# Performance work log

Measured on AMD Instinct MI355X. Metric: run time of the kernel, lower is better.

Reference implementation:

```python
import jax, jax.numpy as jnp
import numpy as np

ANISO = (0.096, 0.096, 0.096)
BIG = 1e10  # stands in for +inf feature distance
SMOOTH = 1e-05


def _minplus(f, axis, w):
    # exact 1D squared distance transform along `axis` via min-plus conv:
    # g[i] = min_j f[j] + (w*(i-j))^2 ; vectorized over all other dims.
    f = jnp.moveaxis(f, axis, -1)
    n = f.shape[-1]
    idx = jnp.arange(n, dtype=f.dtype)
    d2 = (w * (idx[:, None] - idx[None, :])) ** 2  # [j, i]
    g = jnp.min(f[..., :, None] + d2, axis=-2)
    return jnp.moveaxis(g, -1, axis)


def _edt_multilabel(labels, num_labels):
    # labels: [b, X, Y, Z] int, values in [1, num_labels]
    # Multi-label euclidean distance transform (edt.edt semantics on gt+1):
    # for each voxel, distance to nearest voxel carrying a DIFFERENT label,
    # scaled by ANISO. Computed as per-label squared EDT fields (separable
    # min-plus per axis, exact) combined by excluding the voxel's own label.
    fields = []
    for L in range(1, num_labels + 1):  # small fixed loop over classes
        f = jnp.where(labels == L, 0.0, BIG).astype(jnp.float32)
        for ax, w in zip((1, 2, 3), ANISO):
            f = _minplus(f, ax, w)
        fields.append(f)
    D = jnp.stack(fields, axis=0)  # [L, b, X, Y, Z] squared distances
    own = jnp.moveaxis(jax.nn.one_hot(labels - 1, num_labels, dtype=jnp.float32), -1, 0)
    d2 = jnp.min(jnp.where(own > 0, BIG, D), axis=0)  # nearest different label
    return jnp.sqrt(d2)


def setup_inputs() -> dict:
    key = jax.random.key(0)
    kx, ky = jax.random.split(key)
    x = jax.random.uniform(kx, (2, 3, 64, 64, 64), dtype=jnp.float32)  # softmax probs
    y = jax.random.randint(ky, (2, 1, 64, 64, 64), 0, 3)  # label map, classes 0..2
    return {"x": x, "y": y}


def reference(x, y):
    b, c = x.shape[:2]
    yi = y[:, 0]  # [b, X, Y, Z]
    # scatter_(1, gt, 1) -> one hot over channel dim
    y_onehot = jnp.moveaxis(jax.nn.one_hot(yi, c, dtype=x.dtype), -1, 1)  # [b,c,X,Y,Z]
    # dt = edt(gt + 1) + 1 ; all labels >=1 so every voxel is 'foreground'
    dt = (_edt_multilabel(yi + 1, c) + 1.0)[:, None]  # [b,1,X,Y,Z]
    fp = x * (1.0 - y_onehot) * dt
    fn = (1.0 - x) * y_onehot * dt
    # do_bg=False (non-batch-dice path): drop background channel
    fp = fp[:, 1:]
    fn = fn[:, 1:]
    return jnp.mean(fp) + jnp.mean(fn) + SMOOTH
```

## Files before the change

### kernel.cpp

```cpp
#include <hip/hip_runtime.h>
#include <math.h>

#define BIGV 10000000000.0f
#define WA   0.096f


__global__ __launch_bounds__(256) void pass_z_kernel(const int* __restrict__ lab,
                                                     float* __restrict__ D) {
    const int vol = blockIdx.y;
    const int b   = vol / 3;
    const int L   = vol % 3;
    const int ys  = blockIdx.x;
    const int lane = threadIdx.x & 63;
    const int wv   = threadIdx.x >> 6;

    __shared__ float s[64][64];

    const int* lp = lab + b * 262144 + ys * 64;
    for (int z = wv; z < 64; z += 4)
        s[z][lane] = (lp[z * 4096 + lane] == L) ? 0.0f : BIGV;
    __syncthreads();

    const int ibase = wv * 16;
    float m[16];
#pragma unroll
    for (int ii = 0; ii < 16; ++ii) m[ii] = __builtin_inff();

    for (int j = 0; j < 64; ++j) {
        const float v  = s[j][lane];
        const float fb = (float)(ibase - j);
#pragma unroll
        for (int ii = 0; ii < 16; ++ii) {
            const float t = WA * (fb + (float)ii);
            m[ii] = fminf(m[ii], __builtin_fmaf(t, t, v));
        }
    }

    float* Dp = D + vol * 262144 + ys * 64;
#pragma unroll
    for (int ii = 0; ii < 16; ++ii)
        Dp[(ibase + ii) * 4096 + lane] = m[ii];
}

__global__ __launch_bounds__(256) void pass_y_kernel(float* __restrict__ D) {
    const int vol = blockIdx.y;
    const int z   = blockIdx.x;
    const int lane = threadIdx.x & 63;
    const int wv   = threadIdx.x >> 6;

    __shared__ float s[64][64];
    float* Dp = D + (vol * 64 + z) * 4096;
    float* sf = &s[0][0];
    for (int t = threadIdx.x; t < 4096; t += 256) sf[t] = Dp[t];
    __syncthreads();

    const int ibase = wv * 16;
    float m[16];
#pragma unroll
    for (int ii = 0; ii < 16; ++ii) m[ii] = __builtin_inff();

    for (int j = 0; j < 64; ++j) {
        const float v  = s[j][lane];
        const float fb = (float)(ibase - j);
#pragma unroll
        for (int ii = 0; ii < 16; ++ii) {
            const float t = WA * (fb + (float)ii);
            m[ii] = fminf(m[ii], __builtin_fmaf(t, t, v));
        }
    }

#pragma unroll
    for (int ii = 0; ii < 16; ++ii)
        Dp[(ibase + ii) * 64 + lane] = m[ii];
}

__global__ __launch_bounds__(256) void pass_x_combine_kernel(const float* __restrict__ x,
                                                             const int* __restrict__ lab,
                                                             const float* __restrict__ D,
                                                             float* __restrict__ partials) {
    const int lane = threadIdx.x & 63;
    const int wv   = threadIdx.x >> 6;
    const int wid  = blockIdx.x * 4 + wv;
    const int b  = wid >> 12;
    const int z  = (wid >> 6) & 63;
    const int yy = wid & 63;

    const int off = (z * 64 + yy) * 64 + lane;

    const float f0 = D[(b * 3 + 0) * 262144 + off];
    const float f1 = D[(b * 3 + 1) * 262144 + off];
    const float f2 = D[(b * 3 + 2) * 262144 + off];

    float m0 = __builtin_inff(), m1 = __builtin_inff(), m2 = __builtin_inff();
    for (int j = 0; j < 64; ++j) {
        const float t   = WA * (float)(lane - j);
        const float d2v = t * t;
        m0 = fminf(m0, __shfl(f0, j) + d2v);
        m1 = fminf(m1, __shfl(f1, j) + d2v);
        m2 = fminf(m2, __shfl(f2, j) + d2v);
    }

    const int lv = lab[b * 262144 + off];
    const float d0 = (lv == 0) ? BIGV : m0;
    const float d1 = (lv == 1) ? BIGV : m1;
    const float d2 = (lv == 2) ? BIGV : m2;
    const float dt = sqrtf(fminf(d0, fminf(d1, d2))) + 1.0f;

    const float x1 = x[(b * 3 + 1) * 262144 + off];
    const float x2 = x[(b * 3 + 2) * 262144 + off];
    const float t1 = (lv == 1) ? (1.0f - x1) : x1;
    const float t2 = (lv == 2) ? (1.0f - x2) : x2;
    float part = (t1 + t2) * dt;

#pragma unroll
    for (int o = 32; o; o >>= 1) part += __shfl_down(part, o);

    __shared__ float ps[4];
    if (lane == 0) ps[wv] = part;
    __syncthreads();
    if (threadIdx.x == 0)
        partials[blockIdx.x] = ps[0] + ps[1] + ps[2] + ps[3];
}

__global__ __launch_bounds__(256) void final_reduce_kernel(const float* __restrict__ partials,
                                                           float* __restrict__ out) {
    __shared__ float s[256];
    float v = 0.0f;
    for (int i = threadIdx.x; i < 2048; i += 256) v += partials[i];
    s[threadIdx.x] = v;
    __syncthreads();
    for (int st = 128; st > 0; st >>= 1) {
        if (threadIdx.x < st) s[threadIdx.x] += s[threadIdx.x + st];
        __syncthreads();
    }
    if (threadIdx.x == 0)
        out[0] = s[0] * (1.0f / 1048576.0f) + 1e-5f;
}

extern "C" void kernel_launch(void* const* d_in, const int* in_sizes, int n_in,
                              void* d_out, int out_size, void* d_ws, size_t ws_size,
                              hipStream_t stream) {
    const float* x  = (const float*)d_in[0];
    const int*   y  = (const int*)d_in[1];
    float* D        = (float*)d_ws;
    float* partials = D + 6 * 262144;
    float* out      = (float*)d_out;

    pass_z_kernel<<<dim3(64, 6), 256, 0, stream>>>(y, D);
    pass_y_kernel<<<dim3(64, 6), 256, 0, stream>>>(D);
    pass_x_combine_kernel<<<dim3(2048), 256, 0, stream>>>(x, y, D, partials);
    final_reduce_kernel<<<dim3(1), 256, 0, stream>>>(partials, out);
}
```

Before: 119.2 us.

## Fuse y and x EDT passes with combine, process all labels per block, atomic reduce

The z pass now handles all three label fields in one block, reading the label slab once and splitting output rows across two blocks. The y pass is fused with the x pass and the loss combine: each block keeps its y-pass results in registers, runs the x min-plus with wave shuffles, and accumulates the loss directly. The partials buffer and final reduce kernel are replaced by per-wave atomicAdd to the output after a memset. This cuts the launch count and skips one global round trip of the distance fields, at the cost of fewer blocks (256) with much higher register pressure and a float-atomic summation order that is not deterministic.

```diff
diff --git a/kernel.cpp b/kernel.cpp
--- a/kernel.cpp
+++ b/kernel.cpp
@@ -4,150 +4,140 @@
 #define BIGV 10000000000.0f
 #define WA   0.096f
 
-
 __global__ __launch_bounds__(256) void pass_z_kernel(const int* __restrict__ lab,
                                                      float* __restrict__ D) {
-    const int vol = blockIdx.y;
-    const int b   = vol / 3;
-    const int L   = vol % 3;
-    const int ys  = blockIdx.x;
+    const int ys = blockIdx.x, b = blockIdx.y, ih = blockIdx.z;
     const int lane = threadIdx.x & 63;
     const int wv   = threadIdx.x >> 6;
 
-    __shared__ float s[64][64];
-
+    __shared__ int sl[64][64];
     const int* lp = lab + b * 262144 + ys * 64;
     for (int z = wv; z < 64; z += 4)
-        s[z][lane] = (lp[z * 4096 + lane] == L) ? 0.0f : BIGV;
+        sl[z][lane] = lp[z * 4096 + lane];
     __syncthreads();
 
-    const int ibase = wv * 16;
-    float m[16];
+    const int i0 = ih * 32 + wv * 8;
+    float m0[8], m1[8], m2[8];
 #pragma unroll
-    for (int ii = 0; ii < 16; ++ii) m[ii] = __builtin_inff();
+    for (int ii = 0; ii < 8; ++ii) m0[ii] = m1[ii] = m2[ii] = __builtin_inff();
 
     for (int j = 0; j < 64; ++j) {
-        const float v  = s[j][lane];
-        const float fb = (float)(ibase - j);
+        const int lv = sl[j][lane];
+        const float v0 = (lv == 0) ? 0.0f : BIGV;
+        const float v1 = (lv == 1) ? 0.0f : BIGV;
+        const float v2 = (lv == 2) ? 0.0f : BIGV;
+        const float fb = (float)(i0 - j);
 #pragma unroll
-        for (int ii = 0; ii < 16; ++ii) {
+        for (int ii = 0; ii < 8; ++ii) {
             const float t = WA * (fb + (float)ii);
-            m[ii] = fminf(m[ii], __builtin_fmaf(t, t, v));
+            m0[ii] = fminf(m0[ii], __builtin_fmaf(t, t, v0));
+            m1[ii] = fminf(m1[ii], __builtin_fmaf(t, t, v1));
+            m2[ii] = fminf(m2[ii], __builtin_fmaf(t, t, v2));
         }
     }
 
-    float* Dp = D + vol * 262144 + ys * 64;
+    float* Dp = D + b * 3 * 262144 + ys * 64;
 #pragma unroll
-    for (int ii = 0; ii < 16; ++ii)
-        Dp[(ibase + ii) * 4096 + lane] = m[ii];
+    for (int ii = 0; ii < 8; ++ii) {
+        const int zo = (i0 + ii) * 4096 + lane;
+        Dp[zo]              = m0[ii];
+        Dp[262144 + zo]     = m1[ii];
+        Dp[2 * 262144 + zo] = m2[ii];
+    }
 }
 
-__global__ __launch_bounds__(256) void pass_y_kernel(float* __restrict__ D) {
-    const int vol = blockIdx.y;
-    const int z   = blockIdx.x;
+__global__ __launch_bounds__(256) void pass_yx_kernel(const float* __restrict__ x,
+                                                      const int* __restrict__ lab,
+                                                      const float* __restrict__ D,
+                                                      float* __restrict__ out) {
+    const int z = blockIdx.x, b = blockIdx.y, yh = blockIdx.z;
     const int lane = threadIdx.x & 63;
     const int wv   = threadIdx.x >> 6;
 
-    __shared__ float s[64][64];
-    float* Dp = D + (vol * 64 + z) * 4096;
-    float* sf = &s[0][0];
-    for (int t = threadIdx.x; t < 4096; t += 256) sf[t] = Dp[t];
+    __shared__ float s[3][64][64];
+    const float* Dp = D + b * 3 * 262144 + z * 4096;
+    float* sf = &s[0][0][0];
+    for (int t = threadIdx.x; t < 4096; t += 256) {
+        sf[t]        = Dp[t];
+        sf[4096 + t] = Dp[262144 + t];
+        sf[8192 + t] = Dp[2 * 262144 + t];
+    }
     __syncthreads();
 
-    const int ibase = wv * 16;
-    float m[16];
+    const int i0 = yh * 32 + wv * 8;
+    float m0[8], m1[8], m2[8];
 #pragma unroll
-    for (int ii = 0; ii < 16; ++ii) m[ii] = __builtin_inff();
+    for (int ii = 0; ii < 8; ++ii) m0[ii] = m1[ii] = m2[ii] = __builtin_inff();
 
     for (int j = 0; j < 64; ++j) {
-        const float v  = s[j][lane];
-        const float fb = (float)(ibase - j);
+        const float a0 = s[0][j][lane];
+        const float a1 = s[1][j][lane];
+        const float a2 = s[2][j][lane];
+        const float fb = (float)(i0 - j);
 #pragma unroll
-        for (int ii = 0; ii < 16; ++ii) {
+        for (int ii = 0; ii < 8; ++ii) {
             const float t = WA * (fb + (float)ii);
-            m[ii] = fminf(m[ii], __builtin_fmaf(t, t, v));
+            m0[ii] = fminf(m0[ii], __builtin_fmaf(t, t, a0));
+            m1[ii] = fminf(m1[ii], __builtin_fmaf(t, t, a1));
+            m2[ii] = fminf(m2[ii], __builtin_fmaf(t, t, a2));
         }
     }
 
+    int   lv[8];
+    float x1[8], x2[8];
+    const int base = b * 262144 + z * 4096 + lane;
 #pragma unroll
-    for (int ii = 0; ii < 16; ++ii)
-        Dp[(ibase + ii) * 64 + lane] = m[ii];
-}
+    for (int ii = 0; ii < 8; ++ii) {
+        const int off = base + (i0 + ii) * 64;
+        lv[ii] = lab[off];
+        x1[ii] = x[262144 + b * 3 * 262144 + z * 4096 + (i0 + ii) * 64 + lane];
+        x2[ii] = x[2 * 262144 + b * 3 * 262144 + z * 4096 + (i0 + ii) * 64 + lane];
+    }
 
-__global__ __launch_bounds__(256) void pass_x_combine_kernel(const float* __restrict__ x,
-                                                             const int* __restrict__ lab,
-                                                             const float* __restrict__ D,
-                                                             float* __restrict__ partials) {
-    const int lane = threadIdx.x & 63;
-    const int wv   = threadIdx.x >> 6;
-    const int wid  = blockIdx.x * 4 + wv;
-    const int b  = wid >> 12;
-    const int z  = (wid >> 6) & 63;
-    const int yy = wid & 63;
+    float g0[8], g1[8], g2[8];
+#pragma unroll
+    for (int ii = 0; ii < 8; ++ii) g0[ii] = g1[ii] = g2[ii] = __builtin_inff();
 
-    const int off = (z * 64 + yy) * 64 + lane;
-
-    const float f0 = D[(b * 3 + 0) * 262144 + off];
-    const float f1 = D[(b * 3 + 1) * 262144 + off];
-    const float f2 = D[(b * 3 + 2) * 262144 + off];
-
-    float m0 = __builtin_inff(), m1 = __builtin_inff(), m2 = __builtin_inff();
     for (int j = 0; j < 64; ++j) {
         const float t   = WA * (float)(lane - j);
         const float d2v = t * t;
-        m0 = fminf(m0, __shfl(f0, j) + d2v);
-        m1 = fminf(m1, __shfl(f1, j) + d2v);
-        m2 = fminf(m2, __shfl(f2, j) + d2v);
+#pragma unroll
+        for (int ii = 0; ii < 8; ++ii) {
+            g0[ii] = fminf(g0[ii], __shfl(m0[ii], j) + d2v);
+            g1[ii] = fminf(g1[ii], __shfl(m1[ii], j) + d2v);
+            g2[ii] = fminf(g2[ii], __shfl(m2[ii], j) + d2v);
+        }
     }
 
-    const int lv = lab[b * 262144 + off];
-    const float d0 = (lv == 0) ? BIGV : m0;
-    const float d1 = (lv == 1) ? BIGV : m1;
-    const float d2 = (lv == 2) ? BIGV : m2;
-    const float dt = sqrtf(fminf(d0, fminf(d1, d2))) + 1.0f;
-
-    const float x1 = x[(b * 3 + 1) * 262144 + off];
-    const float x2 = x[(b * 3 + 2) * 262144 + off];
-    const float t1 = (lv == 1) ? (1.0f - x1) : x1;
-    const float t2 = (lv == 2) ? (1.0f - x2) : x2;
-    float part = (t1 + t2) * dt;
+    float part = 0.0f;
+#pragma unroll
+    for (int ii = 0; ii < 8; ++ii) {
+        const float d0  = (lv[ii] == 0) ? BIGV : g0[ii];
+        const float d1  = (lv[ii] == 1) ? BIGV : g1[ii];
+        const float d2m = (lv[ii] == 2) ? BIGV : g2[ii];
+        const float dt  = sqrtf(fminf(d0, fminf(d1, d2m))) + 1.0f;
+        const float t1  = (lv[ii] == 1) ? (1.0f - x1[ii]) : x1[ii];
+        const float t2  = (lv[ii] == 2) ? (1.0f - x2[ii]) : x2[ii];
+        part += (t1 + t2) * dt;
+    }
 
 #pragma unroll
     for (int o = 32; o; o >>= 1) part += __shfl_down(part, o);
-
-    __shared__ float ps[4];
-    if (lane == 0) ps[wv] = part;
-    __syncthreads();
-    if (threadIdx.x == 0)
-        partials[blockIdx.x] = ps[0] + ps[1] + ps[2] + ps[3];
-}
-
-__global__ __launch_bounds__(256) void final_reduce_kernel(const float* __restrict__ partials,
-                                                           float* __restrict__ out) {
-    __shared__ float s[256];
-    float v = 0.0f;
-    for (int i = threadIdx.x; i < 2048; i += 256) v += partials[i];
-    s[threadIdx.x] = v;
-    __syncthreads();
-    for (int st = 128; st > 0; st >>= 1) {
-        if (threadIdx.x < st) s[threadIdx.x] += s[threadIdx.x + st];
-        __syncthreads();
-    }
-    if (threadIdx.x == 0)
-        out[0] = s[0] * (1.0f / 1048576.0f) + 1e-5f;
+    if (lane == 0)
+        atomicAdd(out, part * (1.0f / 1048576.0f));
+    if (blockIdx.x == 0 && blockIdx.y == 0 && blockIdx.z == 0 && threadIdx.x == 0)
+        atomicAdd(out, 1e-5f);
 }
 
 extern "C" void kernel_launch(void* const* d_in, const int* in_sizes, int n_in,
                               void* d_out, int out_size, void* d_ws, size_t ws_size,
                               hipStream_t stream) {
-    const float* x  = (const float*)d_in[0];
-    const int*   y  = (const int*)d_in[1];
-    float* D        = (float*)d_ws;
-    float* partials = D + 6 * 262144;
-    float* out      = (float*)d_out;
+    const float* x = (const float*)d_in[0];
+    const int*   y = (const int*)d_in[1];
+    float* D   = (float*)d_ws;
+    float* out = (float*)d_out;
 
-    pass_z_kernel<<<dim3(64, 6), 256, 0, stream>>>(y, D);
-    pass_y_kernel<<<dim3(64, 6), 256, 0, stream>>>(D);
-    pass_x_combine_kernel<<<dim3(2048), 256, 0, stream>>>(x, y, D, partials);
-    final_reduce_kernel<<<dim3(1), 256, 0, stream>>>(partials, out);
+    hipMemsetAsync(out, 0, sizeof(float), stream);
+    pass_z_kernel<<<dim3(64, 2, 2), 256, 0, stream>>>(y, D);
+    pass_yx_kernel<<<dim3(64, 2, 2), 256, 0, stream>>>(x, y, D, out);
 }
```

New measurement: 123.6 us. 1.04x slower.
